# Kernel optimization log

Measured on AMD Instinct MI355X. Metric: run time of the kernel, lower is better.

The kernel has to match this reference:

```python
import jax, jax.numpy as jnp
import numpy as np

WINDOW_SIZE = 11
NUM_BINS = 256
SIGMA = 1.5
C1 = 0.01 ** 2
C2 = 0.03 ** 2
MAX_PSNR = 40.0


def _gaussian_window():
    xs = jnp.arange(WINDOW_SIZE, dtype=jnp.float32)
    g = jnp.exp(-((xs - WINDOW_SIZE // 2) ** 2) / (2.0 * SIGMA ** 2))
    g = g / g.sum()
    w2 = jnp.outer(g, g)  # [11,11]
    return jnp.broadcast_to(w2[None, None], (3, 1, WINDOW_SIZE, WINDOW_SIZE))


def setup_inputs() -> dict:
    key = jax.random.key(0)
    k1, k2 = jax.random.split(key)
    B, C, H, W = 64, 3, 256, 256
    x = jax.random.uniform(k1, (B, C, H, W), dtype=jnp.float32) * 2.0 - 1.0
    y = jax.random.uniform(k2, (B, C, H, W), dtype=jnp.float32) * 2.0 - 1.0
    return {"x": x, "y": y, "window": _gaussian_window()}


def _depthwise_conv(img, w):
    pad = WINDOW_SIZE // 2
    return jax.lax.conv_general_dilated(
        img, w, window_strides=(1, 1), padding=[(pad, pad), (pad, pad)],
        feature_group_count=img.shape[1],
        dimension_numbers=("NCHW", "OIHW", "NCHW"))


def _mi(x, y):
    B = x.shape[0]
    nb = NUM_BINS
    xf = (x.reshape(B, -1) + 1.0) * 0.5  # [B, N] in [0,1]
    yf = (y.reshape(B, -1) + 1.0) * 0.5
    N = xf.shape[1]
    ix = jnp.clip((xf * nb).astype(jnp.int32), 0, nb - 1)
    iy = jnp.clip((yf * nb).astype(jnp.int32), 0, nb - 1)
    flat = (jnp.arange(B, dtype=jnp.int32)[:, None] * (nb * nb) + ix * nb + iy).reshape(-1)
    hist = jnp.zeros(B * nb * nb, jnp.float32).at[flat].add(1.0).reshape(B, nb, nb)
    jp = hist / N  # joint probs [B, nb, nb]
    px = jp.sum(axis=2)  # [B, nb]
    py = jp.sum(axis=1)

    def ent(p):
        return -jnp.sum(jnp.where(p > 0, p * jnp.log2(jnp.where(p > 0, p, 1.0)), 0.0), axis=-1)

    hx = ent(px)
    hy = ent(py)
    pxy = px[:, :, None] * py[:, None, :]
    ratio = jp / jnp.where(pxy > 0, pxy, 1.0)
    mi = jnp.sum(jnp.where(jp > 0, jp * jnp.log2(jnp.where(jp > 0, ratio, 1.0)), 0.0), axis=(1, 2))
    norm = jnp.minimum(hx, hy)  # mi_method='min'
    mi = jnp.where(norm > 0, mi / norm, 0.0)
    return jnp.clip(mi, 0.0, 1.0)


def _ssim(x, y, window):
    mu1 = _depthwise_conv(x, window)
    mu2 = _depthwise_conv(y, window)
    mu1_sq = mu1 * mu1
    mu2_sq = mu2 * mu2
    mu1_mu2 = mu1 * mu2
    sigma1_sq = _depthwise_conv(x * x, window) - mu1_sq
    sigma2_sq = _depthwise_conv(y * y, window) - mu2_sq
    sigma12 = _depthwise_conv(x * y, window) - mu1_mu2
    ssim_map = ((2 * mu1_mu2 + C1) * (2 * sigma12 + C2)) / ((mu1_sq + mu2_sq + C1) * (sigma1_sq + sigma2_sq + C2))
    return ssim_map.mean(axis=(1, 2, 3))


def _psnr(x, y):
    xr = x * 0.5 + 0.5
    yr = y * 0.5 + 0.5
    mse = jnp.mean((xr - yr) ** 2, axis=(1, 2, 3))
    zero = mse == 0
    mse = jnp.where(zero, 1e-8, mse)
    psnr = -10.0 * jnp.log10(mse)  # 20*log10(1.0) == 0
    return jnp.where(zero, 100.0, psnr) / MAX_PSNR


def reference(x, y, window):
    mi_vals = _mi(x, y)
    ssim_vals = _ssim(x, y, window)
    psnr_vals = _psnr(x, y)
    metrics = jnp.stack([mi_vals, ssim_vals, psnr_vals], axis=1)  # [B,3]
    return metrics[:, :, None]  # [B,3,1]
```

## Files before the change

kernel.cpp:

```cpp
#include <hip/hip_runtime.h>
#include <cstdint>
#include <cstddef>

#define BATCH 64
#define CH 3
#define HH 256
#define WW 256
#define NBINS 256
#define NPB (CH*HH*WW)
#define QPX (NPB/4)
#define NHB 256
#define NZ (BATCH*CH)
#define NBANDS 8
#define NCB (NZ*NBANDS)

__device__ __forceinline__ float block_reduce_256(float v, float* buf4) {
    #pragma unroll
    for (int o = 32; o > 0; o >>= 1) v += __shfl_down(v, o, 64);
    __syncthreads();
    int lane = threadIdx.x & 63;
    int wid  = threadIdx.x >> 6;
    if (lane == 0) buf4[wid] = v;
    __syncthreads();
    return buf4[0] + buf4[1] + buf4[2] + buf4[3];
}

__device__ __forceinline__ float block_reduce_1024(float v, float* buf16) {
    #pragma unroll
    for (int o = 32; o > 0; o >>= 1) v += __shfl_down(v, o, 64);
    __syncthreads();
    int lane = threadIdx.x & 63;
    int wid  = threadIdx.x >> 6;
    if (lane == 0) buf16[wid] = v;
    __syncthreads();
    float s = 0.0f;
    #pragma unroll
    for (int i = 0; i < 16; i++) s += buf16[i];
    return s;
}

__global__ __launch_bounds__(256) void mega_kernel(
    const float* __restrict__ x, const float* __restrict__ y,
    const float* __restrict__ win,
    float* __restrict__ ssim_partials,
    unsigned int* __restrict__ u4hist, float* __restrict__ mse_part)
{
    __shared__ __align__(16) unsigned char smem[32768];
    const int bid = blockIdx.x;
    const int tid = threadIdx.x;

    if (bid < NHB) {
        unsigned int* h32 = (unsigned int*)smem;
        uint4* h128 = (uint4*)h32;
        #pragma unroll
        for (int i = 0; i < 8; i++) h128[tid + i * 256] = make_uint4(0, 0, 0, 0);
        __syncthreads();

        const int b = bid >> 2, e = bid & 3;
        const float4* x4 = (const float4*)x + (size_t)b * (NPB/4) + (size_t)e * (QPX/4);
        const float4* y4 = (const float4*)y + (size_t)b * (NPB/4) + (size_t)e * (QPX/4);
        float mse_s = 0.0f;
        for (int i = 0; i < 48; i++) {
            float4 xv = x4[tid + i * 256];
            float4 yv = y4[tid + i * 256];
            float xs[4] = {xv.x, xv.y, xv.z, xv.w};
            float ys[4] = {yv.x, yv.y, yv.z, yv.w};
            #pragma unroll
            for (int q = 0; q < 4; q++) {
                float xc = xs[q], yc = ys[q];
                float d = xc - yc;
                mse_s += d * d;
                int ix = (int)(((xc + 1.0f) * 0.5f) * 256.0f);
                int iy = (int)(((yc + 1.0f) * 0.5f) * 256.0f);
                ix = min(max(ix, 0), 255);
                iy = min(max(iy, 0), 255);
                int key = ix * NBINS + iy;
                atomicAdd(&h32[key >> 3], 1u << (4 * (key & 7)));
            }
        }
        #pragma unroll
        for (int o = 32; o > 0; o >>= 1) mse_s += __shfl_down(mse_s, o, 64);
        if ((tid & 63) == 0) mse_part[bid * 4 + (tid >> 6)] = mse_s;
        __syncthreads();

        #pragma unroll
        for (int k = 0; k < 32; k++)
            u4hist[(size_t)bid * 8192 + tid + k * 256] = h32[tid + k * 256];
        return;
    }

    float* wbuf = (float*)smem;
    float* rbuf = (float*)(smem + 5120);

    const int cb = bid - NHB;
    const int z = cb >> 3, band = cb & 7;
    const int w = tid >> 6, l = tid & 63;
    float* wb = wbuf + w * 320;

    const float* xi = x + (size_t)z * (HH * WW);
    const float* yi = y + (size_t)z * (HH * WW);

    float g0, g1, g2, g3, g4, g5, g6, g7, g8, g9, g10;
    {
        float gs = sqrtf(win[60]);
        g0 = win[55] / gs;  g1 = win[56] / gs;  g2 = win[57] / gs;
        g3 = win[58] / gs;  g4 = win[59] / gs;  g5 = win[60] / gs;
        g6 = win[61] / gs;  g7 = win[62] / gs;  g8 = win[63] / gs;
        g9 = win[64] / gs;  g10 = win[65] / gs;
    }

    const int r0g = band * 32 - 5;
    const int gc  = tid - 5;
    const int gc2 = gc + 64;
    const bool okc  = (gc >= 0);
    const bool okc2 = (gc2 < WW);

#define RING_DECL(F) float F##0=0.f,F##1=0.f,F##2=0.f,F##3=0.f,F##4=0.f, \
    F##5=0.f,F##6=0.f,F##7=0.f,F##8=0.f,F##9=0.f,F##10=0.f
    RING_DECL(aX); RING_DECL(aY); RING_DECL(aU); RING_DECL(aV);

    {
        int gr = r0g;
        bool okr = (gr >= 0) && (gr < HH);
        const float* xr = xi + gr * WW;
        const float* yr = yi + gr * WW;
        float xv = (okr && okc) ? xr[gc] : 0.0f;
        float yv = (okr && okc) ? yr[gc] : 0.0f;
        wb[l]      = xv;
        wb[80 + l] = yv;
        if (l < 10) {
            float xv2 = (okr && okc2) ? xr[gc2] : 0.0f;
            float yv2 = (okr && okc2) ? yr[gc2] : 0.0f;
            wb[l + 64]      = xv2;
            wb[80 + l + 64] = yv2;
        }
    }

    float ssim_s = 0.0f;
    const float C1v = 1e-4f, C2v = 9e-4f;
    #pragma unroll 1
    for (int r = 0; r < 42; ++r) {
        const int p = r & 1;
        float* cur = wb + p * 160;
        if (r < 41) {
            int gr = r0g + r + 1;
            bool okr = (gr >= 0) && (gr < HH);
            const float* xr = xi + gr * WW;
            const float* yr = yi + gr * WW;
            float xv = (okr && okc) ? xr[gc] : 0.0f;
            float yv = (okr && okc) ? yr[gc] : 0.0f;
            float* nxt = wb + (p ^ 1) * 160;
            nxt[l]      = xv;
            nxt[80 + l] = yv;
            if (l < 10) {
                float xv2 = (okr && okc2) ? xr[gc2] : 0.0f;
                float yv2 = (okr && okc2) ? yr[gc2] : 0.0f;
                nxt[l + 64]      = xv2;
                nxt[80 + l + 64] = yv2;
            }
        }
        float hx = 0.0f, hy = 0.0f, hu = 0.0f, hv = 0.0f;
#define HTAP(K, GK) { \
            float a  = cur[l + K]; \
            float b2 = cur[80 + l + K]; \
            hx = fmaf(GK, a, hx); \
            hy = fmaf(GK, b2, hy); \
            float uu = fmaf(b2, b2, a * a); \
            hu = fmaf(GK, uu, hu); \
            float vv = a * b2; \
            hv = fmaf(GK, vv, hv); }
        HTAP(0, g0)  HTAP(1, g1)  HTAP(2, g2)  HTAP(3, g3)  HTAP(4, g4)
        HTAP(5, g5)  HTAP(6, g6)  HTAP(7, g7)  HTAP(8, g8)  HTAP(9, g9)
        HTAP(10, g10)
#undef HTAP
#define RUPD(J, W) aX##J = fmaf(W, hx, aX##J); aY##J = fmaf(W, hy, aY##J); \
                   aU##J = fmaf(W, hu, aU##J); aV##J = fmaf(W, hv, aV##J);
        RUPD(0, g10) RUPD(1, g9) RUPD(2, g8) RUPD(3, g7) RUPD(4, g6)
        RUPD(5, g5)  RUPD(6, g4) RUPD(7, g3) RUPD(8, g2) RUPD(9, g1)
        RUPD(10, g0)
#undef RUPD
        if (r >= 10) {
            float m1 = aX0, m2 = aY0;
            float m1s = m1 * m1, m2s = m2 * m2, m12 = m1 * m2;
            float ssum = aU0 - m1s - m2s;
            float s12  = aV0 - m12;
            float num = (2.0f * m12 + C1v) * (2.0f * s12 + C2v);
            float den = (m1s + m2s + C1v) * (ssum + C2v);
            ssim_s += __fdividef(num, den);
        }
#define RSH(A, B) aX##A = aX##B; aY##A = aY##B; aU##A = aU##B; aV##A = aV##B;
        RSH(0,1) RSH(1,2) RSH(2,3) RSH(3,4) RSH(4,5)
        RSH(5,6) RSH(6,7) RSH(7,8) RSH(8,9) RSH(9,10)
#undef RSH
        aX10 = 0.0f; aY10 = 0.0f; aU10 = 0.0f; aV10 = 0.0f;
    }

    float ssim_b = block_reduce_256(ssim_s, rbuf);
    if (tid == 0)
        ssim_partials[(size_t)z * NBANDS + band] = ssim_b;
}

__global__ __launch_bounds__(1024) void merge_finalize_kernel(
    const unsigned int* __restrict__ u4hist,
    const float* __restrict__ mse_part, const float* __restrict__ ssim_partials,
    float* __restrict__ out)
{
    __shared__ unsigned int colw[16][256];
    __shared__ float rbuf[16];
    const int b = blockIdx.x, t = threadIdx.x;
    const int w = t >> 6, l = t & 63;
    const float invN = 1.0f / (float)NPB;

    #pragma unroll
    for (int i = 0; i < 4; i++) ((unsigned int*)colw)[t + i * 1024] = 0;
    __syncthreads();

    float sxy = 0.0f, sx = 0.0f;
    for (int s = 0; s < 4; s++) {
        unsigned int s0a = 0, s1a = 0, s0b = 0, s1b = 0;
        #pragma unroll
        for (int p = 0; p < 4; p++) {
            const uint2* src = (const uint2*)(u4hist + (size_t)(b * 4 + p) * 8192 + s * 2048);
            uint2 v = src[t];
            s0a += v.x & 0x0F0F0F0Fu;  s1a += (v.x >> 4) & 0x0F0F0F0Fu;
            s0b += v.y & 0x0F0F0F0Fu;  s1b += (v.y >> 4) & 0x0F0F0F0Fu;
        }
        unsigned int cnt[16];
        #pragma unroll
        for (int m = 0; m < 4; m++) {
            cnt[2*m]         = (s0a >> (8*m)) & 255u;
            cnt[2*m + 1]     = (s1a >> (8*m)) & 255u;
            cnt[8 + 2*m]     = (s0b >> (8*m)) & 255u;
            cnt[8 + 2*m + 1] = (s1b >> (8*m)) & 255u;
        }

        unsigned int rowc = 0;
        #pragma unroll
        for (int k = 0; k < 16; k++) {
            unsigned int v = cnt[k];
            rowc += v;
            if (v) {
                float jp = (float)v * invN;
                sxy += jp * __log2f(jp);
            }
        }
        #pragma unroll
        for (int o = 8; o > 0; o >>= 1) rowc += __shfl_xor((int)rowc, o, 16);
        if ((t & 15) == 0 && rowc) {
            float px = (float)rowc * invN;
            sx += px * __log2f(px);
        }

        #pragma unroll
        for (int k = 0; k < 16; k++) {
            cnt[k] += __shfl_xor((int)cnt[k], 16, 64);
            cnt[k] += __shfl_xor((int)cnt[k], 32, 64);
        }
        if (l < 16) {
            #pragma unroll
            for (int k = 0; k < 16; k++) colw[w][16 * l + k] += cnt[k];
        }
    }

    float sxy_blk = block_reduce_1024(sxy, rbuf);
    float sx_blk  = block_reduce_1024(sx, rbuf);

    float ey = 0.0f;
    if (t < 256) {
        unsigned int pc = 0;
        #pragma unroll
        for (int ww = 0; ww < 16; ww++) pc += colw[ww][t];
        if (pc) {
            float py = (float)pc * invN;
            ey = -py * __log2f(py);
        }
    }
    float hy = block_reduce_1024(ey, rbuf);
    float ssim_total = block_reduce_1024(
        (t < 24) ? ssim_partials[(size_t)b * 24 + t] : 0.0f, rbuf);
    float mse_all = block_reduce_1024(
        (t < 16) ? mse_part[b * 16 + t] : 0.0f, rbuf);

    if (t == 0) {
        float hxy = -sxy_blk;
        float hx  = -sx_blk;
        float mi = hx + hy - hxy;
        float norm = fminf(hx, hy);
        float m = (norm > 0.0f) ? (mi / norm) : 0.0f;
        m = fminf(fmaxf(m, 0.0f), 1.0f);
        out[b * 3 + 0] = m;
        out[b * 3 + 1] = ssim_total * invN;
        double mse = (double)mse_all * (1.0 / (4.0 * (double)NPB));
        out[b * 3 + 2] = (mse == 0.0) ? 2.5f : (float)(-10.0 * log10(mse) / 40.0);
    }
}

extern "C" void kernel_launch(void* const* d_in, const int* in_sizes, int n_in,
                              void* d_out, int out_size, void* d_ws, size_t ws_size,
                              hipStream_t stream) {
    const float* x   = (const float*)d_in[0];
    const float* y   = (const float*)d_in[1];
    const float* win = (const float*)d_in[2];
    float* out = (float*)d_out;

    char* p = (char*)d_ws;
    unsigned int* u4hist = (unsigned int*)p;
    size_t off = (size_t)NHB * 8192 * sizeof(unsigned int);
    float* mse_part = (float*)(p + off);        off += (size_t)NHB * 4 * sizeof(float);
    float* ssim_partials = (float*)(p + off);

    mega_kernel<<<dim3(NHB + NCB), dim3(256), 0, stream>>>(
        x, y, win, ssim_partials, u4hist, mse_part);
    merge_finalize_kernel<<<dim3(BATCH), dim3(1024), 0, stream>>>(
        u4hist, mse_part, ssim_partials, out);
}
```

Measured before the change: 216.1 us.

## Double block size to 512 threads and merge two SSIM bands per block

The combined kernel now launches 512-thread blocks. Histogram blocks take half as many loop iterations, and each SSIM block covers two row bands with 8 independent wavefronts. The per-block shared-memory SSIM reduction is replaced by per-wavefront shuffle sums written to a larger partials array, which the finalize kernel then reduces. Row loads now use clamped addresses with a select-to-zero instead of conditional loads. The aim is to cut the SSIM block count and the __syncthreads reductions, at the cost of larger blocks that may hurt occupancy given the 32KB shared allocation.

```diff
diff --git a/kernel.cpp b/kernel.cpp
--- a/kernel.cpp
+++ b/kernel.cpp
@@ -11,19 +11,7 @@
 #define QPX (NPB/4)
 #define NHB 256
 #define NZ (BATCH*CH)
-#define NBANDS 8
-#define NCB (NZ*NBANDS)
-
-__device__ __forceinline__ float block_reduce_256(float v, float* buf4) {
-    #pragma unroll
-    for (int o = 32; o > 0; o >>= 1) v += __shfl_down(v, o, 64);
-    __syncthreads();
-    int lane = threadIdx.x & 63;
-    int wid  = threadIdx.x >> 6;
-    if (lane == 0) buf4[wid] = v;
-    __syncthreads();
-    return buf4[0] + buf4[1] + buf4[2] + buf4[3];
-}
+#define NCB (NZ*4)
 
 __device__ __forceinline__ float block_reduce_1024(float v, float* buf16) {
     #pragma unroll
@@ -39,7 +27,7 @@
     return s;
 }
 
-__global__ __launch_bounds__(256) void mega_kernel(
+__global__ __launch_bounds__(512, 8) void mega_kernel(
     const float* __restrict__ x, const float* __restrict__ y,
     const float* __restrict__ win,
     float* __restrict__ ssim_partials,
@@ -53,16 +41,16 @@
         unsigned int* h32 = (unsigned int*)smem;
         uint4* h128 = (uint4*)h32;
         #pragma unroll
-        for (int i = 0; i < 8; i++) h128[tid + i * 256] = make_uint4(0, 0, 0, 0);
+        for (int i = 0; i < 4; i++) h128[tid + i * 512] = make_uint4(0, 0, 0, 0);
         __syncthreads();
 
         const int b = bid >> 2, e = bid & 3;
         const float4* x4 = (const float4*)x + (size_t)b * (NPB/4) + (size_t)e * (QPX/4);
         const float4* y4 = (const float4*)y + (size_t)b * (NPB/4) + (size_t)e * (QPX/4);
         float mse_s = 0.0f;
-        for (int i = 0; i < 48; i++) {
-            float4 xv = x4[tid + i * 256];
-            float4 yv = y4[tid + i * 256];
+        for (int i = 0; i < 24; i++) {
+            float4 xv = x4[tid + i * 512];
+            float4 yv = y4[tid + i * 512];
             float xs[4] = {xv.x, xv.y, xv.z, xv.w};
             float ys[4] = {yv.x, yv.y, yv.z, yv.w};
             #pragma unroll
@@ -80,21 +68,21 @@
         }
         #pragma unroll
         for (int o = 32; o > 0; o >>= 1) mse_s += __shfl_down(mse_s, o, 64);
-        if ((tid & 63) == 0) mse_part[bid * 4 + (tid >> 6)] = mse_s;
+        if ((tid & 63) == 0) mse_part[bid * 8 + (tid >> 6)] = mse_s;
         __syncthreads();
 
         #pragma unroll
-        for (int k = 0; k < 32; k++)
-            u4hist[(size_t)bid * 8192 + tid + k * 256] = h32[tid + k * 256];
+        for (int k = 0; k < 16; k++)
+            u4hist[(size_t)bid * 8192 + tid + k * 512] = h32[tid + k * 512];
         return;
     }
 
     float* wbuf = (float*)smem;
-    float* rbuf = (float*)(smem + 5120);
-
     const int cb = bid - NHB;
-    const int z = cb >> 3, band = cb & 7;
+    const int z = cb >> 2, bp = cb & 3;
     const int w = tid >> 6, l = tid & 63;
+    const int seg  = w & 3;
+    const int band = bp * 2 + (w >> 2);
     float* wb = wbuf + w * 320;
 
     const float* xi = x + (size_t)z * (HH * WW);
@@ -110,55 +98,53 @@
     }
 
     const int r0g = band * 32 - 5;
-    const int gc  = tid - 5;
+    const int gc  = seg * 64 + l - 5;
     const int gc2 = gc + 64;
     const bool okc  = (gc >= 0);
     const bool okc2 = (gc2 < WW);
+    const int c1 = okc ? gc : 0;
+    const int c2 = okc2 ? gc2 : 0;
+
+#define LOADROW(GR, RX0, RY0, RX1, RY1) { \
+        int gr_ = (GR); \
+        bool okr_ = (gr_ >= 0) && (gr_ < HH); \
+        int grc_ = min(max(gr_, 0), HH - 1); \
+        const float* xr_ = xi + grc_ * WW; \
+        const float* yr_ = yi + grc_ * WW; \
+        RX0 = xr_[c1]; RY0 = yr_[c1]; \
+        if (!(okr_ && okc)) { RX0 = 0.0f; RY0 = 0.0f; } \
+        if (l < 10) { \
+            RX1 = xr_[c2]; RY1 = yr_[c2]; \
+            if (!(okr_ && okc2)) { RX1 = 0.0f; RY1 = 0.0f; } \
+        } }
+#define WRITEROW(PAR, RX0, RY0, RX1, RY1) { \
+        float* dst_ = wb + (PAR) * 160; \
+        dst_[l] = RX0; dst_[80 + l] = RY0; \
+        if (l < 10) { dst_[64 + l] = RX1; dst_[80 + 64 + l] = RY1; } }
 
 #define RING_DECL(F) float F##0=0.f,F##1=0.f,F##2=0.f,F##3=0.f,F##4=0.f, \
     F##5=0.f,F##6=0.f,F##7=0.f,F##8=0.f,F##9=0.f,F##10=0.f
     RING_DECL(aX); RING_DECL(aY); RING_DECL(aU); RING_DECL(aV);
 
     {
-        int gr = r0g;
-        bool okr = (gr >= 0) && (gr < HH);
-        const float* xr = xi + gr * WW;
-        const float* yr = yi + gr * WW;
-        float xv = (okr && okc) ? xr[gc] : 0.0f;
-        float yv = (okr && okc) ? yr[gc] : 0.0f;
-        wb[l]      = xv;
-        wb[80 + l] = yv;
-        if (l < 10) {
-            float xv2 = (okr && okc2) ? xr[gc2] : 0.0f;
-            float yv2 = (okr && okc2) ? yr[gc2] : 0.0f;
-            wb[l + 64]      = xv2;
-            wb[80 + l + 64] = yv2;
-        }
-    }
+        float px0, py0, px1 = 0.0f, py1 = 0.0f;
+        LOADROW(r0g, px0, py0, px1, py1);
+        WRITEROW(0, px0, py0, px1, py1);
+    }
+    asm volatile("" ::: "memory");
 
     float ssim_s = 0.0f;
     const float C1v = 1e-4f, C2v = 9e-4f;
     #pragma unroll 1
     for (int r = 0; r < 42; ++r) {
-        const int p = r & 1;
-        float* cur = wb + p * 160;
         if (r < 41) {
-            int gr = r0g + r + 1;
-            bool okr = (gr >= 0) && (gr < HH);
-            const float* xr = xi + gr * WW;
-            const float* yr = yi + gr * WW;
-            float xv = (okr && okc) ? xr[gc] : 0.0f;
-            float yv = (okr && okc) ? yr[gc] : 0.0f;
-            float* nxt = wb + (p ^ 1) * 160;
-            nxt[l]      = xv;
-            nxt[80 + l] = yv;
-            if (l < 10) {
-                float xv2 = (okr && okc2) ? xr[gc2] : 0.0f;
-                float yv2 = (okr && okc2) ? yr[gc2] : 0.0f;
-                nxt[l + 64]      = xv2;
-                nxt[80 + l + 64] = yv2;
-            }
-        }
+            float nx0 = 0.0f, ny0 = 0.0f, nx1 = 0.0f, ny1 = 0.0f;
+            LOADROW(r0g + r + 1, nx0, ny0, nx1, ny1);
+            WRITEROW((r + 1) & 1, nx0, ny0, nx1, ny1);
+        }
+        asm volatile("" ::: "memory");
+
+        float* cur = wb + (r & 1) * 160;
         float hx = 0.0f, hy = 0.0f, hu = 0.0f, hv = 0.0f;
 #define HTAP(K, GK) { \
             float a  = cur[l + K]; \
@@ -194,10 +180,12 @@
 #undef RSH
         aX10 = 0.0f; aY10 = 0.0f; aU10 = 0.0f; aV10 = 0.0f;
     }
-
-    float ssim_b = block_reduce_256(ssim_s, rbuf);
-    if (tid == 0)
-        ssim_partials[(size_t)z * NBANDS + band] = ssim_b;
+#undef LOADROW
+#undef WRITEROW
+
+    #pragma unroll
+    for (int o = 32; o > 0; o >>= 1) ssim_s += __shfl_down(ssim_s, o, 64);
+    if (l == 0) ssim_partials[(size_t)cb * 8 + w] = ssim_s;
 }
 
 __global__ __launch_bounds__(1024) void merge_finalize_kernel(
@@ -277,9 +265,9 @@
     }
     float hy = block_reduce_1024(ey, rbuf);
     float ssim_total = block_reduce_1024(
-        (t < 24) ? ssim_partials[(size_t)b * 24 + t] : 0.0f, rbuf);
+        (t < 96) ? ssim_partials[(size_t)b * 96 + t] : 0.0f, rbuf);
     float mse_all = block_reduce_1024(
-        (t < 16) ? mse_part[b * 16 + t] : 0.0f, rbuf);
+        (t < 32) ? mse_part[b * 32 + t] : 0.0f, rbuf);
 
     if (t == 0) {
         float hxy = -sxy_blk;
@@ -306,10 +294,10 @@
     char* p = (char*)d_ws;
     unsigned int* u4hist = (unsigned int*)p;
     size_t off = (size_t)NHB * 8192 * sizeof(unsigned int);
-    float* mse_part = (float*)(p + off);        off += (size_t)NHB * 4 * sizeof(float);
+    float* mse_part = (float*)(p + off);        off += (size_t)NHB * 8 * sizeof(float);
     float* ssim_partials = (float*)(p + off);
 
-    mega_kernel<<<dim3(NHB + NCB), dim3(256), 0, stream>>>(
+    mega_kernel<<<dim3(NHB + NCB), dim3(512), 0, stream>>>(
         x, y, win, ssim_partials, u4hist, mse_part);
     merge_finalize_kernel<<<dim3(BATCH), dim3(1024), 0, stream>>>(
         u4hist, mse_part, ssim_partials, out);
```

After: 729.6 us. 3.38x slower.
